# Kernel optimization log

Measured on AMD Instinct MI355X. Metric: run time of the kernel, lower is better.

Reference implementation:

```python
import jax, jax.numpy as jnp
import numpy as np
import math

K_DIM = 1024
HEADS = 16

def setup_inputs() -> dict:
    key = jax.random.key(0)
    ks = jax.random.split(key, 6)
    b, N, k = 4, 2048, K_DIM
    sc = 1.0 / math.sqrt(k)
    return {
        "x": jax.random.normal(ks[0], (b, N, k), dtype=jnp.float32),
        "Wk": jax.random.normal(ks[1], (k, k), dtype=jnp.float32) * sc,
        "Wq": jax.random.normal(ks[2], (k, k), dtype=jnp.float32) * sc,
        "Wv": jax.random.normal(ks[3], (k, k), dtype=jnp.float32) * sc,
        "Wu": jax.random.normal(ks[4], (k, k), dtype=jnp.float32) * sc,
        "bu": jax.random.normal(ks[5], (k,), dtype=jnp.float32) * 0.01,
    }

def reference(x, Wk, Wq, Wv, Wu, bu):
    b, N, k = x.shape
    h = HEADS
    s = k // h
    # torch Linear: y = x @ W^T
    Q = (x @ Wq.T).reshape(b, N, h, s).transpose(0, 2, 1, 3)  # [b,h,N,s]
    Kh = (x @ Wk.T).reshape(b, N, h, s).transpose(0, 2, 1, 3)
    V = (x @ Wv.T).reshape(b, N, h, s).transpose(0, 2, 1, 3)
    scores = jnp.einsum('bhid,bhjd->bhij', Q, Kh) / math.sqrt(s)  # [b,h,N,N]
    attn = jax.nn.softmax(scores, axis=-1)
    out = jnp.einsum('bhij,bhjd->bhid', attn, V)  # [b,h,N,s]
    out = out.transpose(0, 2, 1, 3).reshape(b, N, k)
    return out @ Wu.T + bu
```

## Files before the change

### kernel.cpp

```cpp
#include <hip/hip_runtime.h>

typedef __bf16 bf16;
typedef __bf16 bf16x4 __attribute__((ext_vector_type(4)));
typedef __bf16 bf16x8 __attribute__((ext_vector_type(8)));
typedef float  f32x4  __attribute__((ext_vector_type(4)));

#define MFMA16(a, b, c) __builtin_amdgcn_mfma_f32_16x16x32_bf16((a), (b), (c), 0, 0, 0)

__device__ __forceinline__ void async_copy16(const void* g, void* l) {
  __builtin_amdgcn_global_load_lds(
      (const __attribute__((address_space(1))) unsigned int*)g,
      (__attribute__((address_space(3))) unsigned int*)l, 16, 0, 0);
}

struct CvtArgs {
  const float* src[5];
  bf16* dst[5];
  int blk_start[6];
};
__global__ void k_cvt_all(CvtArgs a) {
  int b = blockIdx.x;
  int seg = 0;
#pragma unroll
  for (int s = 1; s < 5; ++s) seg += (b >= a.blk_start[s]);
  int i = (b - a.blk_start[seg]) * 1024 + threadIdx.x * 4;
  float4 v = *(const float4*)(a.src[seg] + i);
  bf16x4 o = { (bf16)v.x, (bf16)v.y, (bf16)v.z, (bf16)v.w };
  *(bf16x4*)(a.dst[seg] + i) = o;
}

template <int OUTF32>
__device__ __forceinline__ void gemm128_body(
    const bf16* __restrict__ A, const bf16* __restrict__ B, void* __restrict__ Cp,
    const float* __restrict__ bias, int m0, int n0, int N, int K) {
  __shared__ alignas(16) bf16 As[128 * 32];
  __shared__ alignas(16) bf16 Bs[128 * 32];
  const int tid = threadIdx.x;
  const int lane = tid & 63;
  const int w = tid >> 6;
  const int quad = lane >> 4;
  const int l16 = lane & 15;
  const int wr = (w >> 1) * 64;
  const int wc = (w & 1) * 64;

  const int srow = tid >> 2;
  const int skk = (tid & 3) * 8;
  const bf16* Ag = A + (long)(m0 + srow) * K + skk;
  const bf16* Bg = B + (long)(n0 + srow) * K + skk;
  const long half = 64L * K;
  bf16* AsW = As + w * 512;
  bf16* BsW = Bs + w * 512;

  f32x4 acc[4][4];
#pragma unroll
  for (int i = 0; i < 4; ++i)
#pragma unroll
    for (int j = 0; j < 4; ++j) acc[i][j] = (f32x4){0.f, 0.f, 0.f, 0.f};

  for (int k0 = 0; k0 < K; k0 += 32) {
    async_copy16(Ag + k0, AsW);
    async_copy16(Ag + half + k0, AsW + 2048);
    async_copy16(Bg + k0, BsW);
    async_copy16(Bg + half + k0, BsW + 2048);
    __syncthreads();
    bf16x8 af[4], bfr[4];
#pragma unroll
    for (int i = 0; i < 4; ++i)
      af[i] = *(const bf16x8*)&As[(wr + i * 16 + l16) * 32 + quad * 8];
#pragma unroll
    for (int j = 0; j < 4; ++j)
      bfr[j] = *(const bf16x8*)&Bs[(wc + j * 16 + l16) * 32 + quad * 8];
#pragma unroll
    for (int i = 0; i < 4; ++i)
#pragma unroll
      for (int j = 0; j < 4; ++j) acc[i][j] = MFMA16(af[i], bfr[j], acc[i][j]);
    __syncthreads();
  }

#pragma unroll
  for (int i = 0; i < 4; ++i)
#pragma unroll
    for (int j = 0; j < 4; ++j)
#pragma unroll
      for (int r = 0; r < 4; ++r) {
        long row = m0 + wr + i * 16 + quad * 4 + r;
        int col = n0 + wc + j * 16 + l16;
        if (OUTF32)
          ((float*)Cp)[row * N + col] = acc[i][j][r] + bias[col];
        else
          ((bf16*)Cp)[row * N + col] = (bf16)acc[i][j][r];
      }
}

__global__ __launch_bounds__(256) void k_gemm_qkv(
    const bf16* __restrict__ xb, const bf16* __restrict__ Wqk, bf16* __restrict__ QKb,
    const bf16* __restrict__ Wvb, bf16* __restrict__ VtG) {
  int bid = blockIdx.x;
  if (bid < 1024) {
    int bm = bid & 63, bn = bid >> 6;
    gemm128_body<0>(xb, Wqk, QKb, nullptr, bm * 128, bn * 128, 2048, 1024);
  } else {
    int id = bid - 1024;
    int bm = id & 7, bn = id >> 3;
    gemm128_body<0>(Wvb, xb, VtG, nullptr, bm * 128, bn * 128, 8192, 1024);
  }
}

__global__ __launch_bounds__(256) void k_gemm_out(
    const bf16* __restrict__ Ab, const bf16* __restrict__ Wub, float* __restrict__ out,
    const float* __restrict__ bu) {
  gemm128_body<1>(Ab, Wub, out, bu, blockIdx.x * 128, blockIdx.y * 128, 1024, 1024);
}

__global__ __launch_bounds__(256) void k_attn(
    const bf16* __restrict__ Q, const bf16* __restrict__ Kb,
    const bf16* __restrict__ Vt, bf16* __restrict__ O) {
  __shared__ alignas(16) bf16 Ps[128][72];
  __shared__ alignas(16) bf16 Ks[64][72];
  __shared__ alignas(16) bf16 Vs[64][72];

  const int tid = threadIdx.x;
  const int lane = tid & 63;
  const int w = tid >> 6;
  const int quad = lane >> 4;
  const int l16 = lane & 15;
  const int qt = blockIdx.x;
  const int bh = blockIdx.y;
  const int bb = bh >> 4;
  const int h = bh & 15;
  const int hoff = h * 64;
  const long rowQ0 = (long)bb * 2048 + qt * 128;
  const long kv0 = (long)bb * 2048;

  {
    int r = tid >> 1;
    int c0 = (tid & 1) * 32;
    const bf16* p = Q + (rowQ0 + r) * 2048 + hoff + c0;
#pragma unroll
    for (int u = 0; u < 4; ++u) {
      bf16x8 v = *(const bf16x8*)(p + u * 8);
      bf16x8 o;
#pragma unroll
      for (int j = 0; j < 8; ++j) o[j] = (bf16)((float)v[j] * 0.125f);
      *(bf16x8*)&Ps[r][c0 + u * 8] = o;
    }
  }
  bf16x8 bq[2][2];
#pragma unroll
  for (int g = 0; g < 2; ++g)
#pragma unroll
    for (int ss = 0; ss < 2; ++ss)
      bq[g][ss] = *(const bf16x8*)&Ps[w * 32 + g * 16 + l16][ss * 32 + quad * 8];

  f32x4 accO[2][4];
  float lp[2] = {0.f, 0.f};
#pragma unroll
  for (int g = 0; g < 2; ++g)
#pragma unroll
    for (int t = 0; t < 4; ++t) accO[g][t] = (f32x4){0.f, 0.f, 0.f, 0.f};

  const int srow = tid >> 2;
  const int scol = (tid & 3) * 8;
  const bf16* kp = Kb + (kv0 + srow) * 2048 + hoff + scol;
  const bf16* vp = Vt + (long)(hoff + srow) * 8192 + kv0 + scol;

  bf16x8 kr0 = *(const bf16x8*)kp;
  bf16x8 kr1 = *(const bf16x8*)(kp + 32);
  bf16x8 vr0 = *(const bf16x8*)vp;
  bf16x8 vr1 = *(const bf16x8*)(vp + 32);

  for (int kt = 0; kt < 32; ++kt) {
    __syncthreads();
    *(bf16x8*)&Ks[srow][scol] = kr0;
    *(bf16x8*)&Ks[srow][scol + 32] = kr1;
    *(bf16x8*)&Vs[srow][scol] = vr0;
    *(bf16x8*)&Vs[srow][scol + 32] = vr1;
    __syncthreads();
    if (kt < 31) {
      const bf16* kp2 = kp + (long)(kt + 1) * 64 * 2048;
      const bf16* vp2 = vp + (kt + 1) * 64;
      kr0 = *(const bf16x8*)kp2;
      kr1 = *(const bf16x8*)(kp2 + 32);
      vr0 = *(const bf16x8*)vp2;
      vr1 = *(const bf16x8*)(vp2 + 32);
    }

    f32x4 st[2][4];
#pragma unroll
    for (int g = 0; g < 2; ++g)
#pragma unroll
      for (int mt = 0; mt < 4; ++mt) st[g][mt] = (f32x4){0.f, 0.f, 0.f, 0.f};
#pragma unroll
    for (int mt = 0; mt < 4; ++mt) {
      bf16x8 ak0 = *(const bf16x8*)&Ks[mt * 16 + l16][quad * 8];
      bf16x8 ak1 = *(const bf16x8*)&Ks[mt * 16 + l16][32 + quad * 8];
      st[0][mt] = MFMA16(ak0, bq[0][0], st[0][mt]);
      st[0][mt] = MFMA16(ak1, bq[0][1], st[0][mt]);
      st[1][mt] = MFMA16(ak0, bq[1][0], st[1][mt]);
      st[1][mt] = MFMA16(ak1, bq[1][1], st[1][mt]);
    }

#pragma unroll
    for (int g = 0; g < 2; ++g)
#pragma unroll
      for (int mt = 0; mt < 4; ++mt) {
        bf16x4 pk;
#pragma unroll
        for (int r = 0; r < 4; ++r) {
          float pv = __expf(st[g][mt][r]);
          lp[g] += pv;
          pk[r] = (bf16)pv;
        }
        *(bf16x4*)&Ps[w * 32 + g * 16 + l16][mt * 16 + quad * 4] = pk;
      }

#pragma unroll
    for (int ss = 0; ss < 2; ++ss) {
      bf16x8 ap0 = *(const bf16x8*)&Ps[w * 32 + l16][ss * 32 + quad * 8];
      bf16x8 ap1 = *(const bf16x8*)&Ps[w * 32 + 16 + l16][ss * 32 + quad * 8];
#pragma unroll
      for (int t = 0; t < 4; ++t) {
        bf16x8 bv = *(const bf16x8*)&Vs[t * 16 + l16][ss * 32 + quad * 8];
        accO[0][t] = MFMA16(ap0, bv, accO[0][t]);
        accO[1][t] = MFMA16(ap1, bv, accO[1][t]);
      }
    }
  }

  float linv[2];
#pragma unroll
  for (int g = 0; g < 2; ++g) {
    float l = lp[g];
    l += __shfl_xor(l, 16);
    l += __shfl_xor(l, 32);
    linv[g] = 1.f / l;
  }
#pragma unroll
  for (int g = 0; g < 2; ++g)
#pragma unroll
    for (int r = 0; r < 4; ++r) {
      float inv = __shfl(linv[g], (lane & 48) | (quad * 4 + r));
      long row = rowQ0 + w * 32 + g * 16 + quad * 4 + r;
#pragma unroll
      for (int t = 0; t < 4; ++t)
        O[row * 1024 + hoff + t * 16 + l16] = (bf16)(accO[g][t][r] * inv);
    }
}

extern "C" void kernel_launch(void* const* d_in, const int* in_sizes, int n_in,
                              void* d_out, int out_size, void* d_ws, size_t ws_size,
                              hipStream_t stream) {
  const float* x  = (const float*)d_in[0];
  const float* Wk = (const float*)d_in[1];
  const float* Wq = (const float*)d_in[2];
  const float* Wv = (const float*)d_in[3];
  const float* Wu = (const float*)d_in[4];
  const float* bu = (const float*)d_in[5];
  float* out = (float*)d_out;

  const int XE = 4 * 2048 * 1024;
  const int WE = 1024 * 1024;

  bf16* p = (bf16*)d_ws;
  bf16* xb   = p; p += XE;
  bf16* Wqkb = p; p += 2 * WE;
  bf16* Wvb  = p; p += WE;
  bf16* Wub  = p; p += WE;
  bf16* QKb  = p; p += 2 * XE;
  bf16* VtG  = p; p += XE;
  bf16* Ab   = p; p += XE;

  CvtArgs ca;
  ca.src[0] = x;  ca.dst[0] = xb;
  ca.src[1] = Wq; ca.dst[1] = Wqkb;
  ca.src[2] = Wk; ca.dst[2] = Wqkb + WE;
  ca.src[3] = Wv; ca.dst[3] = Wvb;
  ca.src[4] = Wu; ca.dst[4] = Wub;
  ca.blk_start[0] = 0;
  ca.blk_start[1] = XE / 1024;
  ca.blk_start[2] = ca.blk_start[1] + WE / 1024;
  ca.blk_start[3] = ca.blk_start[2] + WE / 1024;
  ca.blk_start[4] = ca.blk_start[3] + WE / 1024;
  ca.blk_start[5] = ca.blk_start[4] + WE / 1024;
  k_cvt_all<<<ca.blk_start[5], 256, 0, stream>>>(ca);

  k_gemm_qkv<<<1536, 256, 0, stream>>>(xb, Wqkb, QKb, Wvb, VtG);

  k_attn<<<dim3(16, 64), 256, 0, stream>>>(QKb, QKb + 1024, VtG, Ab);

  k_gemm_out<<<dim3(64, 8), 256, 0, stream>>>(Ab, Wub, out, bu);
}
```

Baseline: 284.9 us.

## Double attention query tile to 256 rows per block and hoist K/V fragment loads

Each attention block now handles 256 query rows, 64 per wave, instead of 128, so every K/V tile loaded into shared memory is reused by twice as many queries. The grid shrinks to 8x64 blocks. K and V MFMA fragments are read from LDS once per tile into registers and reused across four row groups, with the score/exp/PV steps interleaved per group. This cuts global and LDS traffic per query but raises register pressure (more accumulators), doubles the P buffer in LDS, and halves the block count to 512, which may reduce occupancy and load balance; launch_bounds(256,2) is added to limit register use.

Measured after the change: 265.2 us. -6.9%, faster.

```diff
diff --git a/kernel.cpp b/kernel.cpp
--- a/kernel.cpp
+++ b/kernel.cpp
@@ -112,10 +112,10 @@
   gemm128_body<1>(Ab, Wub, out, bu, blockIdx.x * 128, blockIdx.y * 128, 1024, 1024);
 }
 
-__global__ __launch_bounds__(256) void k_attn(
+__global__ __launch_bounds__(256, 2) void k_attn(
     const bf16* __restrict__ Q, const bf16* __restrict__ Kb,
     const bf16* __restrict__ Vt, bf16* __restrict__ O) {
-  __shared__ alignas(16) bf16 Ps[128][72];
+  __shared__ alignas(16) bf16 Ps[256][72];
   __shared__ alignas(16) bf16 Ks[64][72];
   __shared__ alignas(16) bf16 Vs[64][72];
 
@@ -129,33 +129,31 @@
   const int bb = bh >> 4;
   const int h = bh & 15;
   const int hoff = h * 64;
-  const long rowQ0 = (long)bb * 2048 + qt * 128;
+  const long rowQ0 = (long)bb * 2048 + qt * 256;
   const long kv0 = (long)bb * 2048;
 
   {
-    int r = tid >> 1;
-    int c0 = (tid & 1) * 32;
-    const bf16* p = Q + (rowQ0 + r) * 2048 + hoff + c0;
-#pragma unroll
-    for (int u = 0; u < 4; ++u) {
+    const bf16* p = Q + (rowQ0 + tid) * 2048 + hoff;
+#pragma unroll
+    for (int u = 0; u < 8; ++u) {
       bf16x8 v = *(const bf16x8*)(p + u * 8);
       bf16x8 o;
 #pragma unroll
       for (int j = 0; j < 8; ++j) o[j] = (bf16)((float)v[j] * 0.125f);
-      *(bf16x8*)&Ps[r][c0 + u * 8] = o;
-    }
-  }
-  bf16x8 bq[2][2];
-#pragma unroll
-  for (int g = 0; g < 2; ++g)
+      *(bf16x8*)&Ps[tid][u * 8] = o;
+    }
+  }
+  bf16x8 bq[4][2];
+#pragma unroll
+  for (int g = 0; g < 4; ++g)
 #pragma unroll
     for (int ss = 0; ss < 2; ++ss)
-      bq[g][ss] = *(const bf16x8*)&Ps[w * 32 + g * 16 + l16][ss * 32 + quad * 8];
-
-  f32x4 accO[2][4];
-  float lp[2] = {0.f, 0.f};
-#pragma unroll
-  for (int g = 0; g < 2; ++g)
+      bq[g][ss] = *(const bf16x8*)&Ps[w * 64 + g * 16 + l16][ss * 32 + quad * 8];
+
+  f32x4 accO[4][4];
+  float lp[4] = {0.f, 0.f, 0.f, 0.f};
+#pragma unroll
+  for (int g = 0; g < 4; ++g)
 #pragma unroll
     for (int t = 0; t < 4; ++t) accO[g][t] = (f32x4){0.f, 0.f, 0.f, 0.f};
 
@@ -185,66 +183,63 @@
       vr1 = *(const bf16x8*)(vp2 + 32);
     }
 
-    f32x4 st[2][4];
-#pragma unroll
-    for (int g = 0; g < 2; ++g)
-#pragma unroll
-      for (int mt = 0; mt < 4; ++mt) st[g][mt] = (f32x4){0.f, 0.f, 0.f, 0.f};
+    bf16x8 ak[4][2], bv[2][4];
 #pragma unroll
     for (int mt = 0; mt < 4; ++mt) {
-      bf16x8 ak0 = *(const bf16x8*)&Ks[mt * 16 + l16][quad * 8];
-      bf16x8 ak1 = *(const bf16x8*)&Ks[mt * 16 + l16][32 + quad * 8];
-      st[0][mt] = MFMA16(ak0, bq[0][0], st[0][mt]);
-      st[0][mt] = MFMA16(ak1, bq[0][1], st[0][mt]);
-      st[1][mt] = MFMA16(ak0, bq[1][0], st[1][mt]);
-      st[1][mt] = MFMA16(ak1, bq[1][1], st[1][mt]);
-    }
-
-#pragma unroll
-    for (int g = 0; g < 2; ++g)
+      ak[mt][0] = *(const bf16x8*)&Ks[mt * 16 + l16][quad * 8];
+      ak[mt][1] = *(const bf16x8*)&Ks[mt * 16 + l16][32 + quad * 8];
+    }
+#pragma unroll
+    for (int ss = 0; ss < 2; ++ss)
+#pragma unroll
+      for (int t = 0; t < 4; ++t)
+        bv[ss][t] = *(const bf16x8*)&Vs[t * 16 + l16][ss * 32 + quad * 8];
+
+#pragma unroll
+    for (int g = 0; g < 4; ++g) {
+      f32x4 st[4];
+#pragma unroll
+      for (int mt = 0; mt < 4; ++mt) {
+        st[mt] = (f32x4){0.f, 0.f, 0.f, 0.f};
+        st[mt] = MFMA16(ak[mt][0], bq[g][0], st[mt]);
+        st[mt] = MFMA16(ak[mt][1], bq[g][1], st[mt]);
+      }
 #pragma unroll
       for (int mt = 0; mt < 4; ++mt) {
         bf16x4 pk;
 #pragma unroll
         for (int r = 0; r < 4; ++r) {
-          float pv = __expf(st[g][mt][r]);
+          float pv = __expf(st[mt][r]);
           lp[g] += pv;
           pk[r] = (bf16)pv;
         }
-        *(bf16x4*)&Ps[w * 32 + g * 16 + l16][mt * 16 + quad * 4] = pk;
-      }
-
-#pragma unroll
-    for (int ss = 0; ss < 2; ++ss) {
-      bf16x8 ap0 = *(const bf16x8*)&Ps[w * 32 + l16][ss * 32 + quad * 8];
-      bf16x8 ap1 = *(const bf16x8*)&Ps[w * 32 + 16 + l16][ss * 32 + quad * 8];
-#pragma unroll
-      for (int t = 0; t < 4; ++t) {
-        bf16x8 bv = *(const bf16x8*)&Vs[t * 16 + l16][ss * 32 + quad * 8];
-        accO[0][t] = MFMA16(ap0, bv, accO[0][t]);
-        accO[1][t] = MFMA16(ap1, bv, accO[1][t]);
-      }
-    }
-  }
-
-  float linv[2];
-#pragma unroll
-  for (int g = 0; g < 2; ++g) {
+        *(bf16x4*)&Ps[w * 64 + g * 16 + l16][mt * 16 + quad * 4] = pk;
+      }
+#pragma unroll
+      for (int ss = 0; ss < 2; ++ss) {
+        bf16x8 ap = *(const bf16x8*)&Ps[w * 64 + g * 16 + l16][ss * 32 + quad * 8];
+#pragma unroll
+        for (int t = 0; t < 4; ++t)
+          accO[g][t] = MFMA16(ap, bv[ss][t], accO[g][t]);
+      }
+    }
+  }
+
+#pragma unroll
+  for (int g = 0; g < 4; ++g) {
     float l = lp[g];
     l += __shfl_xor(l, 16);
     l += __shfl_xor(l, 32);
-    linv[g] = 1.f / l;
-  }
-#pragma unroll
-  for (int g = 0; g < 2; ++g)
+    float linv = 1.f / l;
 #pragma unroll
     for (int r = 0; r < 4; ++r) {
-      float inv = __shfl(linv[g], (lane & 48) | (quad * 4 + r));
-      long row = rowQ0 + w * 32 + g * 16 + quad * 4 + r;
+      float inv = __shfl(linv, (lane & 48) | (quad * 4 + r));
+      long row = rowQ0 + w * 64 + g * 16 + quad * 4 + r;
 #pragma unroll
       for (int t = 0; t < 4; ++t)
         O[row * 1024 + hoff + t * 16 + l16] = (bf16)(accO[g][t][r] * inv);
     }
+  }
 }
 
 extern "C" void kernel_launch(void* const* d_in, const int* in_sizes, int n_in,
@@ -286,7 +281,7 @@
 
   k_gemm_qkv<<<1536, 256, 0, stream>>>(xb, Wqkb, QKb, Wvb, VtG);
 
-  k_attn<<<dim3(16, 64), 256, 0, stream>>>(QKb, QKb + 1024, VtG, Ab);
+  k_attn<<<dim3(8, 64), 256, 0, stream>>>(QKb, QKb + 1024, VtG, Ab);
 
   k_gemm_out<<<dim3(64, 8), 256, 0, stream>>>(Ab, Wub, out, bu);
 }
```
